# Kernel tuning notes

Measured on AMD Instinct MI355X. Metric: run time of the kernel, lower is better.

Reference implementation:

```python
import jax, jax.numpy as jnp
import numpy as np


def _rosa(x):
    """Suffix-automaton next-symbol predictor, faithful port of rosa() from RWKV-LM.
    x: Python list of ints (binary alphabet 0/1). Returns list y of ints in {-1,0,1}.
    """
    n = len(x)
    y = [-1] * n
    s = 2 * n + 1
    b = [None] * s   # transitions (dict per state)
    c = [-1] * s     # suffix links
    d = [0] * s      # lengths
    e = [-1] * s     # last end-position seen for the state
    b[0] = {}
    g = 0
    z = 1
    for i, t in enumerate(x):
        r = z; z += 1
        b[r] = {}
        d[r] = d[g] + 1
        p = g
        while p != -1 and t not in b[p]:
            b[p][t] = r
            p = c[p]
        if p == -1:
            c[r] = 0
        else:
            q = b[p][t]
            if d[p] + 1 == d[q]:
                c[r] = q
            else:
                u = z; z += 1
                b[u] = b[q].copy()
                d[u] = d[p] + 1
                c[u] = c[q]
                e[u] = e[q]
                while p != -1 and b[p][t] == q:
                    b[p][t] = u
                    p = c[p]
                c[q] = c[r] = u
        v = g = r
        a = -1
        while v != -1:
            if d[v] > 0 and e[v] >= 0:
                a = x[e[v] + 1]
                break
            v = c[v]
        y[i] = a
        v = g
        while v != -1 and e[v] < i:
            e[v] = i
            v = c[v]
    return y


def _rosa_idx(x):
    """Host-side construction of idx[B,T,C] from float input x (bits = x>0).
    The suffix automaton is inherently sequential / data-dependent per (b,c)
    sequence, exactly as in the original module."""
    bits = (np.asarray(x) > 0).astype(np.int64)  # [B,T,C]
    B, T, C = bits.shape
    idx = np.empty((B, T, C), dtype=np.int64)
    for bb in range(B):
        for cc in range(C):
            idx[bb, :, cc] = _rosa(bits[bb, :, cc].tolist())
    return idx


def setup_inputs() -> dict:
    key = jax.random.key(0)
    k1, k2, k3 = jax.random.split(key, 3)
    B, T, C = 2, 2048, 128
    x = jax.random.normal(k1, (B, T, C), dtype=jnp.float32)
    # parameters init'd at +/-1e-5 in the module; use tiny random values of the
    # same scale so the two tables are distinguishable in correctness checks.
    emb0 = jax.random.normal(k2, (1, 1, C), dtype=jnp.float32) * 1e-5
    emb1 = jax.random.normal(k3, (1, 1, C), dtype=jnp.float32) * 1e-5
    return {"x": x, "emb0": emb0, "emb1": emb1}


def reference(x, emb0, emb1):
    # idx in {-1, 0, 1}: predicted next bit after the longest matched suffix
    idx = jnp.asarray(_rosa_idx(x))  # [B,T,C] int64
    e0 = jnp.broadcast_to(emb0, x.shape)
    e1 = jnp.broadcast_to(emb1, x.shape)
    out = jnp.where(idx == -1, jnp.zeros_like(x), jnp.where(idx == 1, e1, e0))
    return out
```

## Files before the change

kernel.cpp:

```cpp
#include <hip/hip_runtime.h>


#define B_   2
#define T_   2048
#define C_   128
#define MAXS 4100

typedef unsigned int       u32;
typedef unsigned short     u16;
typedef unsigned long long u64;
typedef u16 __attribute__((may_alias)) u16a;

__global__ __launch_bounds__(64)
void rosa_kernel(const float* __restrict__ x,
                 const float* __restrict__ emb0,
                 const float* __restrict__ emb1,
                 float* __restrict__ out)
{
    __shared__ u32 tr[MAXS];
    __shared__ u32 el[MAXS];
    __shared__ u64 bits[T_ / 64];
    __shared__ signed char y8[T_];

    const int blk  = blockIdx.x;
    const int bb   = blk >> 7;
    const int cc   = blk & (C_ - 1);
    const int lane = threadIdx.x;

    const float* xp = x + (size_t)bb * T_ * C_ + cc;
    for (int k = 0; k < T_ / 64; ++k) {
        float v = xp[(size_t)(k * 64 + lane) * C_];
        u64 m = __ballot(v > 0.0f);
        if (lane == 0) bits[k] = m;
    }
    __syncthreads();

    u16a* tr16 = (u16a*)tr;
    u16a* el16 = (u16a*)el;

    if (lane == 0) { tr[0] = 0xFFFFFFFFu; el[0] = 0x0000FFFFu; }
    __syncthreads();

    int vch = 0;
    int L   = 1;
    int z   = 1;
    u64 curw = bits[0];
    u64 nxtw = 0;

    for (int i = 0; i < T_; ++i) {
        if ((i & 63) == 0) {
            int w = (i >> 6) + 1;
            nxtw = (w < T_ / 64) ? bits[w] : 0ull;
        }
        const int t  = (int)((curw >> (i & 63)) & 1ull);
        const int sh = t << 4;
        const int r  = z++;

        const bool act = lane < L;
        const u32 trv = tr[vch];
        const u32 elv = el[vch];
        const int qj  = (int)((trv >> sh) & 0xFFFFu);

        const u64 hasmask = __ballot(act && qj != 0xFFFF);
        const bool found  = (hasmask != 0ull);
        const int  k      = found ? (int)__builtin_ctzll(hasmask) : L;

        if (lane < k) tr16[2 * vch + t] = (u16)r;

        const int qe  = (act && qj != 0xFFFF) ? qj : 0;
        const u32 trq = tr[qe];
        const u32 elq = el[qe];
        const int prevq = __shfl_up(qj, 1);

        int u_id  = -1;
        int j_end = k;
        if (found) {
            const int q     = __builtin_amdgcn_readlane(qj, k);
            const u32 elv_k = (u32)__builtin_amdgcn_readlane((int)elv, k);
            const u32 elq_k = (u32)__builtin_amdgcn_readlane((int)elq, k);
            const int len_p = (int)(elv_k >> 16);
            const int len_q = (int)(elq_k >> 16);
            if (len_p + 1 != len_q) {
                u_id = z++;
                const u64 eqm = __ballot(act && qj == q);
                const u64 nq  = (~eqm) >> k;
                const int runlen = nq ? (int)__builtin_ctzll(nq) : (64 - k);
                j_end = k + runlen;
                if (lane >= k && lane < j_end) tr16[2 * vch + t] = (u16)u_id;
                const u32 trq_k = (u32)__builtin_amdgcn_readlane((int)trq, k);
                if (lane == 0) {
                    tr[u_id] = trq_k;
                    el[u_id] = ((u32)(len_p + 1) << 16) | (elq_k & 0xFFFFu);
                }
            }
        }

        const bool part = act && lane >= k;
        const int  img  = (lane < j_end) ? u_id : qj;
        const bool keep = part && (lane == k || lane == j_end ||
                                   (lane > j_end && qj != prevq));
        const u64 keepm = __ballot(keep);
        const int cnt   = __popcll(keepm);
        const int Lnew  = cnt + 2;
        const int pos   = __popcll(keepm & ((1ull << lane) - 1ull));
        const int dest  = keep ? (1 + pos) : 63;
        const u32 pushval = (u32)(img & 0xFFFF) | ((elq & 0xFFFFu) << 16);
        const int perm  = __builtin_amdgcn_ds_permute(dest << 2, (int)pushval);
        const int e_m   = (int)(short)((u32)perm >> 16);

        int a = -1;
        const u64 pmask = __ballot(lane >= 1 && lane < Lnew - 1 && e_m >= 0);
        if (pmask) {
            const int m0 = (int)__builtin_ctzll(pmask);
            const int ev = __builtin_amdgcn_readlane(e_m, m0);
            const int j2 = ev + 1;
            const u64 w  = bits[j2 >> 6];
            a = (int)((w >> (j2 & 63)) & 1ull);
        }
        if (lane == 0) y8[i] = (signed char)a;

        const int vnew = (lane == 0) ? r : ((lane < Lnew - 1) ? (perm & 0xFFFF) : 0);

        if (lane == 0) {
            tr[r] = 0xFFFFFFFFu;
            el[r] = ((u32)(i + 1) << 16) | (u32)(u16)i;
        }
        if (lane >= 1 && lane < Lnew) el16[2 * vnew] = (u16)i;

        vch = vnew;
        L   = Lnew;
        if ((i & 63) == 63) curw = nxtw;
    }
    __syncthreads();

    const float e0 = emb0[cc];
    const float e1 = emb1[cc];
    float* op = out + (size_t)bb * T_ * C_ + cc;
    for (int tt = lane; tt < T_; tt += 64) {
        int yv = y8[tt];
        op[(size_t)tt * C_] = (yv < 0) ? 0.0f : (yv ? e1 : e0);
    }
}

extern "C" void kernel_launch(void* const* d_in, const int* in_sizes, int n_in,
                              void* d_out, int out_size, void* d_ws, size_t ws_size,
                              hipStream_t stream)
{
    const float* x    = (const float*)d_in[0];
    const float* emb0 = (const float*)d_in[1];
    const float* emb1 = (const float*)d_in[2];
    float* out = (float*)d_out;

    dim3 grid(B_ * C_);
    dim3 block(64);
    rosa_kernel<<<grid, block, 0, stream>>>(x, emb0, emb1, out);
}
```

Baseline: 1.275 ms.

## Pack automaton state into 64-bit entries and precompute next-bit per state

```diff
diff --git a/kernel.cpp b/kernel.cpp
--- a/kernel.cpp
+++ b/kernel.cpp
@@ -10,6 +10,7 @@
 typedef unsigned short     u16;
 typedef unsigned long long u64;
 typedef u16 __attribute__((may_alias)) u16a;
+typedef u32 __attribute__((may_alias)) u32a;
 
 __global__ __launch_bounds__(64)
 void rosa_kernel(const float* __restrict__ x,
@@ -17,10 +18,10 @@
                  const float* __restrict__ emb1,
                  float* __restrict__ out)
 {
-    __shared__ u32 tr[MAXS];
-    __shared__ u32 el[MAXS];
+    __shared__ u64 st[MAXS];
     __shared__ u64 bits[T_ / 64];
     __shared__ signed char y8[T_];
+    __shared__ u32 scratch[64];
 
     const int blk  = blockIdx.x;
     const int bb   = blk >> 7;
@@ -35,101 +36,126 @@
     }
     __syncthreads();
 
-    u16a* tr16 = (u16a*)tr;
-    u16a* el16 = (u16a*)el;
+    u16a* tr16 = (u16a*)st;
+    u32a* st32 = (u32a*)st;
 
-    if (lane == 0) { tr[0] = 0xFFFFFFFFu; el[0] = 0x0000FFFFu; }
-    __syncthreads();
+    u64 curw = bits[0];
+    {
+        const int t0 = (int)(curw & 1ull);
+        const int f0 = (int)((curw >> 1) & 1ull);
+        if (lane == 0) {
+            u32 tr0 = 0xFFFFFFFFu & ~(0xFFFFu << (t0 * 16));
+            tr0 |= (1u << (t0 * 16));
+            st[0] = ((u64)((u32)((0 | (f0 << 15)) << 16)) << 32) | tr0;
+            st[1] = ((u64)((u32)((1 | (f0 << 15)) << 16)) << 32) | 0xFFFFFFFFu;
+            y8[0] = (signed char)(-1);
+        }
+    }
 
-    int vch = 0;
-    int L   = 1;
-    int z   = 1;
-    u64 curw = bits[0];
-    u64 nxtw = 0;
+    bool act  = (lane == 63);
+    int  vid  = 0;
+    int  vlen = 0;
+    int  g    = 1;
+    int  z    = 2;
+    u64  nxtw = bits[1];
+    u32  trv  = st32[2 * vid];
 
-    for (int i = 0; i < T_; ++i) {
-        if ((i & 63) == 0) {
-            int w = (i >> 6) + 1;
-            nxtw = (w < T_ / 64) ? bits[w] : 0ull;
-        }
-        const int t  = (int)((curw >> (i & 63)) & 1ull);
+    for (int i = 1; i < T_; ++i) {
+        if ((i & 63) == 0) { curw = nxtw; int w = (i >> 6) + 1; nxtw = (w < T_/64) ? bits[w] : 0ull; }
+        const int ii = i & 63;
+        const int t  = (int)((curw >> ii) & 1ull);
+        const int fb = (ii == 63) ? (int)(nxtw & 1ull) : (int)((curw >> (ii + 1)) & 1ull);
         const int sh = t << 4;
-        const int r  = z++;
 
-        const bool act = lane < L;
-        const u32 trv = tr[vch];
-        const u32 elv = el[vch];
-        const int qj  = (int)((trv >> sh) & 0xFFFFu);
+        const int qj = act ? (int)((trv >> sh) & 0xFFFFu) : 0xFFFF;
+        const u64 hasmask = __ballot(qj != 0xFFFF);
+        const bool found  = hasmask != 0ull;
+        const int  k      = found ? (int)__builtin_ctzll(hasmask) : 64;
+        const int  ks     = k & 63;
 
-        const u64 hasmask = __ballot(act && qj != 0xFFFF);
-        const bool found  = (hasmask != 0ull);
-        const int  k      = found ? (int)__builtin_ctzll(hasmask) : L;
+        const int qe  = (qj == 0xFFFF) ? 0 : qj;
+        const u64 stq = st[qe];
+        const u64 Am  = __ballot(act);
+        const u64 below = Am & ((1ull << lane) - 1ull);
+        const int pidx  = below ? (63 - __builtin_clzll(below)) : 0;
+        const int prevq = __builtin_amdgcn_ds_bpermute(pidx << 2, qj);
 
-        if (lane < k) tr16[2 * vch + t] = (u16)r;
+        const u32 trq = (u32)(stq & 0xFFFFFFFFu);
+        const u32 elq = (u32)(stq >> 32);
+        const int lenq = (int)((elq >> 16) & 0x7FFFu);
 
-        const int qe  = (act && qj != 0xFFFF) ? qj : 0;
-        const u32 trq = tr[qe];
-        const u32 elq = el[qe];
-        const int prevq = __shfl_up(qj, 1);
+        const int q      = __builtin_amdgcn_readlane(qj, ks);
+        const int lenp   = __builtin_amdgcn_readlane(vlen, ks);
+        const int lenq_k = __builtin_amdgcn_readlane(lenq, ks);
+        const u32 elq_k  = (u32)__builtin_amdgcn_readlane((int)elq, ks);
 
-        int u_id  = -1;
-        int j_end = k;
-        if (found) {
-            const int q     = __builtin_amdgcn_readlane(qj, k);
-            const u32 elv_k = (u32)__builtin_amdgcn_readlane((int)elv, k);
-            const u32 elq_k = (u32)__builtin_amdgcn_readlane((int)elq, k);
-            const int len_p = (int)(elv_k >> 16);
-            const int len_q = (int)(elq_k >> 16);
-            if (len_p + 1 != len_q) {
-                u_id = z++;
-                const u64 eqm = __ballot(act && qj == q);
-                const u64 nq  = (~eqm) >> k;
-                const int runlen = nq ? (int)__builtin_ctzll(nq) : (64 - k);
-                j_end = k + runlen;
-                if (lane >= k && lane < j_end) tr16[2 * vch + t] = (u16)u_id;
-                const u32 trq_k = (u32)__builtin_amdgcn_readlane((int)trq, k);
-                if (lane == 0) {
-                    tr[u_id] = trq_k;
-                    el[u_id] = ((u32)(len_p + 1) << 16) | (elq_k & 0xFFFFu);
-                }
-            }
+        const bool clone = found && (lenp + 1 != lenq_k);
+        const int r  = z;
+        const int u_ = z + 1;
+        z += clone ? 2 : 1;
+
+        const u64 aliasm = __ballot(act && lane < k && vid == q);
+        const bool qstale = (q == g) || (aliasm != 0ull);
+
+        const u64 aboveK = ~((2ull << ks) - 1ull);
+        const u64 eqm  = __ballot(qj == q);
+        const u64 badm = Am & ~eqm & aboveK;
+        const int b0   = badm ? (int)__builtin_ctzll(badm) : 64;
+        const bool redir = clone && act && lane >= k && lane < b0 && (qj == q);
+
+        const bool keep = act && lane >= k && (lane == k || qj != prevq);
+        const int id_cand  = (clone && lane == k) ? u_ : qj;
+        const int len_cand = (clone && lane == k) ? (lenp + 1) : lenq;
+        const u64 keepm = __ballot(keep);
+
+        if (act && lane < k) tr16[4 * vid + t] = (u16)r;
+        if (lane == 0)       tr16[4 * g + t]   = (u16)r;
+        if (redir)           tr16[4 * vid + t] = (u16)u_;
+        if (clone && lane == 0) {
+            u32 trqk = (u32)__builtin_amdgcn_readlane((int)trq, ks);
+            if (qstale) trqk = (trqk & ~(0xFFFFu << sh)) | ((u32)r << sh);
+            const u32 w1u = (u32)(u16)i | ((u32)((lenp + 1) | (fb << 15)) << 16);
+            st[u_] = ((u64)w1u << 32) | trqk;
         }
 
-        const bool part = act && lane >= k;
-        const int  img  = (lane < j_end) ? u_id : qj;
-        const bool keep = part && (lane == k || lane == j_end ||
-                                   (lane > j_end && qj != prevq));
-        const u64 keepm = __ballot(keep);
-        const int cnt   = __popcll(keepm);
-        const int Lnew  = cnt + 2;
-        const int pos   = __popcll(keepm & ((1ull << lane) - 1ull));
-        const int dest  = keep ? (1 + pos) : 63;
-        const u32 pushval = (u32)(img & 0xFFFF) | ((elq & 0xFFFFu) << 16);
-        const int perm  = __builtin_amdgcn_ds_permute(dest << 2, (int)pushval);
-        const int e_m   = (int)(short)((u32)perm >> 16);
+        const u32 efv = (u32)(u16)i | ((u32)(len_cand | (fb << 15)) << 16);
+        if (keep) st32[2 * id_cand + 1] = efv;
+        if (lane == 0) {
+            const u32 w1r = (u32)(u16)i | ((u32)((i + 1) | (fb << 15)) << 16);
+            st[r] = ((u64)w1r << 32) | 0xFFFFFFFFu;
+            st32[1] = (u32)(u16)i | ((u32)(0 | (fb << 15)) << 16);
+            const int a = found ? (int)((elq_k >> 31) & 1u) : -1;
+            y8[i] = (signed char)a;
+        }
 
-        int a = -1;
-        const u64 pmask = __ballot(lane >= 1 && lane < Lnew - 1 && e_m >= 0);
-        if (pmask) {
-            const int m0 = (int)__builtin_ctzll(pmask);
-            const int ev = __builtin_amdgcn_readlane(e_m, m0);
-            const int j2 = ev + 1;
-            const u64 w  = bits[j2 >> 6];
-            a = (int)((w >> (j2 & 63)) & 1ull);
+        const bool k63 = (keepm >> 63) & 1ull;
+        const u64  kmid = keepm & 0x7FFFFFFFFFFFFFFFull;
+        const int  P = kmid ? (63 - __builtin_clzll(kmid)) : 0;
+        const int  newpos = P + 1;
+        const bool recomp = k63 && (newpos >= 63);
+
+        bool actn = (keep && lane < 63) || (lane == 63);
+        int  idn  = (keep && lane < 63) ? id_cand : 0;
+        int  lenn = (keep && lane < 63) ? len_cand : 0;
+
+        if (k63 && !recomp) {
+            const int sId  = __builtin_amdgcn_readlane(id_cand, 63);
+            const int sLen = __builtin_amdgcn_readlane(len_cand, 63);
+            if (lane == newpos) { idn = sId; lenn = sLen; actn = true; }
         }
-        if (lane == 0) y8[i] = (signed char)a;
+        if (recomp) {
+            const int dest = 1 + (int)__builtin_popcountll(keepm & ((1ull << lane) - 1ull));
+            if (keep) scratch[dest] = (u32)id_cand | ((u32)len_cand << 16);
+            const int cnt = (int)__builtin_popcountll(keepm);
+            const u32 sc = scratch[lane];
+            const bool inr = (lane >= 1 && lane <= cnt);
+            actn = inr || (lane == 63);
+            idn  = (lane == 63) ? 0 : (inr ? (int)(sc & 0xFFFFu) : 0);
+            lenn = (lane == 63) ? 0 : (inr ? (int)(sc >> 16) : 0);
+        }
 
-        const int vnew = (lane == 0) ? r : ((lane < Lnew - 1) ? (perm & 0xFFFF) : 0);
-
-        if (lane == 0) {
-            tr[r] = 0xFFFFFFFFu;
-            el[r] = ((u32)(i + 1) << 16) | (u32)(u16)i;
-        }
-        if (lane >= 1 && lane < Lnew) el16[2 * vnew] = (u16)i;
-
-        vch = vnew;
-        L   = Lnew;
-        if ((i & 63) == 63) curw = nxtw;
+        act = actn; vid = idn; vlen = lenn; g = r;
+        trv = st32[2 * vid];
     }
     __syncthreads();
 
```

New measurement: 1.073 ms. -15.8%, faster.
